# Optimization experiments

Measured on AMD Instinct MI355X. Metric: run time of the kernel, lower is better.

## Reference

```python
import jax, jax.numpy as jnp
import numpy as np

NEG_INF = -9e15  # same masking constant as the original
LEAKY_ALPHA = 0.2  # tf.nn.leaky_relu default


def setup_inputs() -> dict:
    key = jax.random.key(0)
    k1, k2, k3, k4 = jax.random.split(key, 4)
    N, D, F = 8192, 256, 64
    features = jax.random.normal(k1, (N, D), dtype=jnp.float32)
    adj = jax.random.randint(k2, (N, N), 0, 2, dtype=jnp.int32)
    W = jax.random.normal(k3, (D, F), dtype=jnp.float32) * (1.0 / np.sqrt(D))
    a = jax.random.normal(k4, (2 * F, 1), dtype=jnp.float32) * 0.1
    return {"features": features, "adj": adj, "W": W, "a": a}


def reference(features, adj, W, a):
    # h = X W : [N, F]
    h = features @ W
    F = h.shape[1]
    # a^T [h_i || h_j] = (h a1)_i + (h a2)_j  -- avoids the N*N*2F concat tensor
    a1, a2 = a[:F], a[F:]            # [F,1] each
    e = jax.nn.leaky_relu((h @ a1) + (h @ a2).T, LEAKY_ALPHA)  # [N, N]
    scores = jnp.where(adj > 0, e, jnp.float32(NEG_INF))
    attention = jax.nn.softmax(scores, axis=1)                  # masked softmax over neighbors j
    h_prime = attention @ h                                     # [N, F]
    return jax.nn.elu(h_prime)
```

## Files before the change

kernel.cpp:

```cpp
#include <hip/hip_runtime.h>
#include <hip/hip_bf16.h>
#include <math.h>

#define NN 8192
#define DD 256
#define FF 64
#define WPB 8
#define ROWS 16
#define JW (NN / WPB)
#define CT 128
#define NT (JW / CT)

typedef __attribute__((ext_vector_type(8))) short bf16x8;
typedef __attribute__((ext_vector_type(4))) float f32x4;

__device__ __forceinline__ ushort f2bf(float x) {
  union { __hip_bfloat16 b; ushort s; } u;
  u.b = __float2bfloat16(x);
  return u.s;
}

__global__ __launch_bounds__(256) void k_pre(const float* __restrict__ W,
                                             ushort* __restrict__ WT) {
  const int e4 = (blockIdx.x * 256 + threadIdx.x) * 4;
  const float4 wv = *(const float4*)(W + e4);
  const int k = e4 >> 6, d = e4 & 63;
  WT[(d + 0) * DD + k] = f2bf(wv.x);
  WT[(d + 1) * DD + k] = f2bf(wv.y);
  WT[(d + 2) * DD + k] = f2bf(wv.z);
  WT[(d + 3) * DD + k] = f2bf(wv.w);
}

__global__ __launch_bounds__(256) void k_h(
    const float* __restrict__ feat, const ushort* __restrict__ WT,
    const float* __restrict__ a, ushort* __restrict__ hTf,
    float* __restrict__ E1, float* __restrict__ F1,
    float* __restrict__ E2, float* __restrict__ F2) {
  __shared__ float sp1[4][16], sp2[4][16];
  const int t = threadIdx.x, lane = t & 63, w = t >> 6;
  const int il = lane & 15, kg = lane >> 4;
  const int ibase = blockIdx.x * 16;
  const int d = w * 16 + il;
  const float* frow = feat + (size_t)(ibase + il) * DD + kg * 8;
  const ushort* wrow = WT + (size_t)d * DD + kg * 8;
  f32x4 acc = {0.f, 0.f, 0.f, 0.f};
#pragma unroll
  for (int k0 = 0; k0 < DD; k0 += 32) {
    const float4 fa = *(const float4*)(frow + k0);
    const float4 fb = *(const float4*)(frow + k0 + 4);
    bf16x8 av;
    av[0] = f2bf(fa.x); av[1] = f2bf(fa.y); av[2] = f2bf(fa.z); av[3] = f2bf(fa.w);
    av[4] = f2bf(fb.x); av[5] = f2bf(fb.y); av[6] = f2bf(fb.z); av[7] = f2bf(fb.w);
    const bf16x8 bv = *(const bf16x8*)(wrow + k0);
    acc = __builtin_amdgcn_mfma_f32_16x16x32_bf16(av, bv, acc, 0, 0, 0);
  }
  ushort4 hv;
  hv.x = f2bf(acc[0]);
  hv.y = f2bf(acc[1]);
  hv.z = f2bf(acc[2]);
  hv.w = f2bf(acc[3]);
  {
    const int i0q = ibase + kg * 4;
    const size_t hb = ((size_t)(w * 256 + (i0q >> 5)) * 64 +
                       ((i0q >> 3) & 3) * 16 + il) * 8 + (i0q & 7);
    *(ushort4*)(hTf + hb) = hv;
  }
  const float a1v = a[d], a2v = a[FF + d];
#pragma unroll
  for (int r = 0; r < 4; ++r) {
    float v1 = acc[r] * a1v;
    float v2 = acc[r] * a2v;
#pragma unroll
    for (int m = 1; m <= 8; m <<= 1) {
      v1 += __shfl_xor(v1, m);
      v2 += __shfl_xor(v2, m);
    }
    if (il == 0) {
      sp1[w][kg * 4 + r] = v1;
      sp2[w][kg * 4 + r] = v2;
    }
  }
  __syncthreads();
  if (t < 16) {
    const float s1 = sp1[0][t] + sp1[1][t] + sp1[2][t] + sp1[3][t];
    const float s2 = sp2[0][t] + sp2[1][t] + sp2[2][t] + sp2[3][t];
    E1[ibase + t] = __expf(s1);
    F1[ibase + t] = __expf(0.2f * s1);
    E2[ibase + t] = __expf(s2);
    F2[ibase + t] = __expf(0.2f * s2);
  }
}

__global__ __launch_bounds__(512) void k_attn(
    const int* __restrict__ adj, const ushort* __restrict__ hTf,
    const float* __restrict__ E1g, const float* __restrict__ F1g,
    const float* __restrict__ E2g, const float* __restrict__ F2g,
    float* __restrict__ out) {
  __shared__ __align__(16) char smem[WPB][4480];
  __shared__ float lw[WPB][16];
  const int t = threadIdx.x;
  const int lane = t & 63, w = t >> 6;
  const int il = lane & 15, kg = lane >> 4;
  const int rbase = blockIdx.x * ROWS;
  const int jwin0 = w * JW;
  char* const smemw = smem[w];
  const int arow = lane >> 5;
  const int acol = (lane & 31) * 4;

  float e1p[8], f1p[8];
#pragma unroll
  for (int rep = 0; rep < 8; ++rep) {
    const int r = rbase + rep * 2 + arow;
    e1p[rep] = E1g[r];
    f1p[rep] = F1g[r];
  }
  bf16x8 ones;
#pragma unroll
  for (int e = 0; e < 8; ++e) ones[e] = (short)0x3F80;

  f32x4 acc[4] = {{0,0,0,0},{0,0,0,0},{0,0,0,0},{0,0,0,0}};
  f32x4 accl = {0.f, 0.f, 0.f, 0.f};

  for (int tile = 0; tile < NT; ++tile) {
    const int jt = jwin0 + tile * CT;
    const float4 e2v = *(const float4*)(E2g + jt + acol);
    const float4 f2v = *(const float4*)(F2g + jt + acol);
#pragma unroll
    for (int rep = 0; rep < 8; ++rep) {
      const int r = rep * 2 + arow;
      const int4 av = *(const int4*)(adj + (size_t)(rbase + r) * NN + jt + acol);
      const float e1 = e1p[rep], f1 = f1p[rep];
      float m0 = e1 * e2v.x, m1 = e1 * e2v.y, m2 = e1 * e2v.z, m3 = e1 * e2v.w;
      float p0 = m0 >= 1.f ? m0 : f1 * f2v.x;
      float p1 = m1 >= 1.f ? m1 : f1 * f2v.y;
      float p2 = m2 >= 1.f ? m2 : f1 * f2v.z;
      float p3 = m3 >= 1.f ? m3 : f1 * f2v.w;
      ushort4 pk;
      pk.x = av.x ? f2bf(p0) : (ushort)0;
      pk.y = av.y ? f2bf(p1) : (ushort)0;
      pk.z = av.z ? f2bf(p2) : (ushort)0;
      pk.w = av.w ? f2bf(p3) : (ushort)0;
      const int swz = r * 256 + ((acol * 2) ^ ((r & 7) << 4));
      *(ushort4*)(smemw + swz) = pk;
    }
#pragma unroll
    for (int sb = 0; sb < 4; ++sb) {
      const int coff = (sb * 32 + kg * 8) * 2;
      const bf16x8 pb = *(const bf16x8*)(smemw + il * 256 + (coff ^ ((il & 7) << 4)));
      const int j32 = (jt >> 5) + sb;
      accl = __builtin_amdgcn_mfma_f32_16x16x32_bf16(ones, pb, accl, 0, 0, 0);
#pragma unroll
      for (int f = 0; f < 4; ++f) {
        const bf16x8 hv =
            *(const bf16x8*)(hTf + ((size_t)(f * 256 + j32) * 64 + lane) * 8);
        acc[f] = __builtin_amdgcn_mfma_f32_16x16x32_bf16(hv, pb, acc[f], 0, 0, 0);
      }
    }
  }
  float (*tr)[65] = (float(*)[65])smemw;
#pragma unroll
  for (int f = 0; f < 4; ++f)
#pragma unroll
    for (int r = 0; r < 4; ++r) tr[il][f * 16 + kg * 4 + r] = acc[f][r];
  if (lane < 16) lw[w][il] = accl[0];
  __syncthreads();
#pragma unroll
  for (int k = 0; k < (ROWS * FF) / 512; ++k) {
    const int idx = t + k * 512;
    const int row = idx >> 6, d = idx & 63;
    float s = 0.f, L = 0.f;
#pragma unroll
    for (int ww = 0; ww < WPB; ++ww) {
      s += ((float(*)[65])smem[ww])[row][d];
      L += lw[ww][row];
    }
    const float x = s / fmaxf(L, 1e-30f);
    out[(size_t)(rbase + row) * FF + d] = x > 0.f ? x : expm1f(x);
  }
}

extern "C" void kernel_launch(void* const* d_in, const int* in_sizes, int n_in,
                              void* d_out, int out_size, void* d_ws, size_t ws_size,
                              hipStream_t stream) {
  const float* feat = (const float*)d_in[0];
  const int* adj = (const int*)d_in[1];
  const float* W = (const float*)d_in[2];
  const float* a = (const float*)d_in[3];
  float* out = (float*)d_out;

  ushort* hTf = (ushort*)d_ws;
  ushort* WT = hTf + (size_t)FF * NN;
  float* E1 = (float*)(WT + (size_t)FF * DD);
  float* F1 = E1 + NN;
  float* E2 = F1 + NN;
  float* F2 = E2 + NN;

  hipLaunchKernelGGL(k_pre, dim3(DD * FF / 1024), dim3(256), 0, stream, W, WT);
  hipLaunchKernelGGL(k_h, dim3(NN / 16), dim3(256), 0, stream, feat, WT, a, hTf,
                     E1, F1, E2, F2);
  hipLaunchKernelGGL(k_attn, dim3(NN / ROWS), dim3(512), 0, stream,
                     adj, hTf, E1, F1, E2, F2, out);
}
```

Before: 436.1 us.

## Pack adjacency into a bitmask and build attention operands in registers

```diff
diff --git a/kernel.cpp b/kernel.cpp
--- a/kernel.cpp
+++ b/kernel.cpp
@@ -5,11 +5,9 @@
 #define NN 8192
 #define DD 256
 #define FF 64
-#define WPB 8
+#define WPB 4
 #define ROWS 16
-#define JW (NN / WPB)
-#define CT 128
-#define NT (JW / CT)
+#define CPW (NN / 32 / WPB)
 
 typedef __attribute__((ext_vector_type(8))) short bf16x8;
 typedef __attribute__((ext_vector_type(4))) float f32x4;
@@ -29,6 +27,22 @@
   WT[(d + 1) * DD + k] = f2bf(wv.y);
   WT[(d + 2) * DD + k] = f2bf(wv.z);
   WT[(d + 3) * DD + k] = f2bf(wv.w);
+}
+
+__global__ __launch_bounds__(256) void k_mask(const int* __restrict__ adj,
+                                              uint* __restrict__ mask) {
+  const size_t nquad = (size_t)NN * NN / 4;
+  const size_t stride = (size_t)gridDim.x * 256;
+  const int lane = threadIdx.x & 63;
+  for (size_t q = (size_t)blockIdx.x * 256 + threadIdx.x; q < nquad; q += stride) {
+    const int4 v = ((const int4*)adj)[q];
+    uint nib = (uint)(v.x & 1) | ((uint)(v.y & 1) << 1) |
+               ((uint)(v.z & 1) << 2) | ((uint)(v.w & 1) << 3);
+    uint b = nib | ((uint)__shfl_xor((int)nib, 1) << 4);
+    b |= (uint)__shfl_xor((int)b, 2) << 8;
+    b |= (uint)__shfl_xor((int)b, 4) << 16;
+    if ((lane & 7) == 0) mask[q >> 3] = b;
+  }
 }
 
 __global__ __launch_bounds__(256) void k_h(
@@ -91,29 +105,22 @@
   }
 }
 
-__global__ __launch_bounds__(512) void k_attn(
-    const int* __restrict__ adj, const ushort* __restrict__ hTf,
+__global__ __launch_bounds__(256) void k_attn(
+    const uint* __restrict__ mask, const ushort* __restrict__ hTf,
     const float* __restrict__ E1g, const float* __restrict__ F1g,
     const float* __restrict__ E2g, const float* __restrict__ F2g,
     float* __restrict__ out) {
-  __shared__ __align__(16) char smem[WPB][4480];
+  __shared__ float tr[WPB][16][65];
   __shared__ float lw[WPB][16];
   const int t = threadIdx.x;
   const int lane = t & 63, w = t >> 6;
   const int il = lane & 15, kg = lane >> 4;
   const int rbase = blockIdx.x * ROWS;
-  const int jwin0 = w * JW;
-  char* const smemw = smem[w];
-  const int arow = lane >> 5;
-  const int acol = (lane & 31) * 4;
-
-  float e1p[8], f1p[8];
-#pragma unroll
-  for (int rep = 0; rep < 8; ++rep) {
-    const int r = rbase + rep * 2 + arow;
-    e1p[rep] = E1g[r];
-    f1p[rep] = F1g[r];
-  }
+  const int row = rbase + il;
+  const float e1 = E1g[row], f1 = F1g[row];
+  const uint* mp = mask + (size_t)row * (NN / 32) + w * CPW;
+  const int jb0 = w * CPW * 32 + kg * 8;
+
   bf16x8 ones;
 #pragma unroll
   for (int e = 0; e < 8; ++e) ones[e] = (short)0x3F80;
@@ -121,61 +128,50 @@
   f32x4 acc[4] = {{0,0,0,0},{0,0,0,0},{0,0,0,0},{0,0,0,0}};
   f32x4 accl = {0.f, 0.f, 0.f, 0.f};
 
-  for (int tile = 0; tile < NT; ++tile) {
-    const int jt = jwin0 + tile * CT;
-    const float4 e2v = *(const float4*)(E2g + jt + acol);
-    const float4 f2v = *(const float4*)(F2g + jt + acol);
-#pragma unroll
-    for (int rep = 0; rep < 8; ++rep) {
-      const int r = rep * 2 + arow;
-      const int4 av = *(const int4*)(adj + (size_t)(rbase + r) * NN + jt + acol);
-      const float e1 = e1p[rep], f1 = f1p[rep];
-      float m0 = e1 * e2v.x, m1 = e1 * e2v.y, m2 = e1 * e2v.z, m3 = e1 * e2v.w;
-      float p0 = m0 >= 1.f ? m0 : f1 * f2v.x;
-      float p1 = m1 >= 1.f ? m1 : f1 * f2v.y;
-      float p2 = m2 >= 1.f ? m2 : f1 * f2v.z;
-      float p3 = m3 >= 1.f ? m3 : f1 * f2v.w;
-      ushort4 pk;
-      pk.x = av.x ? f2bf(p0) : (ushort)0;
-      pk.y = av.y ? f2bf(p1) : (ushort)0;
-      pk.z = av.z ? f2bf(p2) : (ushort)0;
-      pk.w = av.w ? f2bf(p3) : (ushort)0;
-      const int swz = r * 256 + ((acol * 2) ^ ((r & 7) << 4));
-      *(ushort4*)(smemw + swz) = pk;
-    }
-#pragma unroll
-    for (int sb = 0; sb < 4; ++sb) {
-      const int coff = (sb * 32 + kg * 8) * 2;
-      const bf16x8 pb = *(const bf16x8*)(smemw + il * 256 + (coff ^ ((il & 7) << 4)));
-      const int j32 = (jt >> 5) + sb;
-      accl = __builtin_amdgcn_mfma_f32_16x16x32_bf16(ones, pb, accl, 0, 0, 0);
-#pragma unroll
-      for (int f = 0; f < 4; ++f) {
-        const bf16x8 hv =
-            *(const bf16x8*)(hTf + ((size_t)(f * 256 + j32) * 64 + lane) * 8);
-        acc[f] = __builtin_amdgcn_mfma_f32_16x16x32_bf16(hv, pb, acc[f], 0, 0, 0);
-      }
-    }
-  }
-  float (*tr)[65] = (float(*)[65])smemw;
+#pragma unroll 4
+  for (int c = 0; c < CPW; ++c) {
+    const uint bits = mp[c] >> (kg * 8);
+    const int jo = jb0 + c * 32;
+    const float4 e2a = *(const float4*)(E2g + jo);
+    const float4 e2b = *(const float4*)(E2g + jo + 4);
+    const float4 f2a = *(const float4*)(F2g + jo);
+    const float4 f2b = *(const float4*)(F2g + jo + 4);
+    bf16x8 pb;
+    pb[0] = (bits & 1u)   ? (short)f2bf(fmaxf(e1 * e2a.x, f1 * f2a.x)) : (short)0;
+    pb[1] = (bits & 2u)   ? (short)f2bf(fmaxf(e1 * e2a.y, f1 * f2a.y)) : (short)0;
+    pb[2] = (bits & 4u)   ? (short)f2bf(fmaxf(e1 * e2a.z, f1 * f2a.z)) : (short)0;
+    pb[3] = (bits & 8u)   ? (short)f2bf(fmaxf(e1 * e2a.w, f1 * f2a.w)) : (short)0;
+    pb[4] = (bits & 16u)  ? (short)f2bf(fmaxf(e1 * e2b.x, f1 * f2b.x)) : (short)0;
+    pb[5] = (bits & 32u)  ? (short)f2bf(fmaxf(e1 * e2b.y, f1 * f2b.y)) : (short)0;
+    pb[6] = (bits & 64u)  ? (short)f2bf(fmaxf(e1 * e2b.z, f1 * f2b.z)) : (short)0;
+    pb[7] = (bits & 128u) ? (short)f2bf(fmaxf(e1 * e2b.w, f1 * f2b.w)) : (short)0;
+    accl = __builtin_amdgcn_mfma_f32_16x16x32_bf16(ones, pb, accl, 0, 0, 0);
+    const int j32 = w * CPW + c;
+#pragma unroll
+    for (int f = 0; f < 4; ++f) {
+      const bf16x8 hv =
+          *(const bf16x8*)(hTf + ((size_t)(f * 256 + j32) * 64 + lane) * 8);
+      acc[f] = __builtin_amdgcn_mfma_f32_16x16x32_bf16(hv, pb, acc[f], 0, 0, 0);
+    }
+  }
 #pragma unroll
   for (int f = 0; f < 4; ++f)
 #pragma unroll
-    for (int r = 0; r < 4; ++r) tr[il][f * 16 + kg * 4 + r] = acc[f][r];
+    for (int r = 0; r < 4; ++r) tr[w][il][f * 16 + kg * 4 + r] = acc[f][r];
   if (lane < 16) lw[w][il] = accl[0];
   __syncthreads();
 #pragma unroll
-  for (int k = 0; k < (ROWS * FF) / 512; ++k) {
-    const int idx = t + k * 512;
-    const int row = idx >> 6, d = idx & 63;
+  for (int k = 0; k < (ROWS * FF) / 256; ++k) {
+    const int idx = t + k * 256;
+    const int r = idx >> 6, d = idx & 63;
     float s = 0.f, L = 0.f;
 #pragma unroll
     for (int ww = 0; ww < WPB; ++ww) {
-      s += ((float(*)[65])smem[ww])[row][d];
-      L += lw[ww][row];
+      s += tr[ww][r][d];
+      L += lw[ww][r];
     }
     const float x = s / fmaxf(L, 1e-30f);
-    out[(size_t)(rbase + row) * FF + d] = x > 0.f ? x : expm1f(x);
+    out[(size_t)(rbase + r) * FF + d] = x > 0.f ? x : expm1f(x);
   }
 }
 
@@ -194,10 +190,12 @@
   float* F1 = E1 + NN;
   float* E2 = F1 + NN;
   float* F2 = E2 + NN;
+  uint* mask = (uint*)(F2 + NN);
 
   hipLaunchKernelGGL(k_pre, dim3(DD * FF / 1024), dim3(256), 0, stream, W, WT);
   hipLaunchKernelGGL(k_h, dim3(NN / 16), dim3(256), 0, stream, feat, WT, a, hTf,
                      E1, F1, E2, F2);
-  hipLaunchKernelGGL(k_attn, dim3(NN / ROWS), dim3(512), 0, stream,
-                     adj, hTf, E1, F1, E2, F2, out);
-}
+  hipLaunchKernelGGL(k_mask, dim3(2048), dim3(256), 0, stream, adj, mask);
+  hipLaunchKernelGGL(k_attn, dim3(NN / ROWS), dim3(256), 0, stream,
+                     mask, hTf, E1, F1, E2, F2, out);
+}
```

After: 442.4 us. Within noise of the previous version (+1.4%).
